# Performance work log

Measured on AMD Instinct MI355X. Metric: run time of the kernel, lower is better.

Reference implementation:

```python
import jax, jax.numpy as jnp
import numpy as np

# module constants (from init_kwargs)
R_EQ = 1.0
WELL_DEPTH = 1.0
CUTOFF = 2.5
HEAL = 0.5

N_EDGES = 20_000_000
N_ATOMS = 1_000_000
N_MOL = 1000


def setup_inputs() -> dict:
    key = jax.random.key(0)
    k1, k2 = jax.random.split(key)
    vec_ij = jax.random.normal(k1, (N_EDGES, 3), dtype=jnp.float32)
    positions = jax.random.normal(k2, (N_ATOMS, 3), dtype=jnp.float32)
    idx_i = jax.random.randint(jax.random.fold_in(key, 1), (N_EDGES,), 0, N_ATOMS, dtype=jnp.int32)
    # sorted molecule indices covering [0, N_MOL), last element == N_MOL-1
    idx_m = (jnp.arange(N_ATOMS, dtype=jnp.int32) * N_MOL // N_ATOMS).astype(jnp.int32)
    return {"vec_ij": vec_ij, "positions": positions, "idx_i": idx_i, "idx_m": idx_m}


def reference(vec_ij, positions, idx_i, idx_m):
    # per-edge distance [E,1]
    r = jnp.linalg.norm(vec_ij, axis=1, keepdims=True)
    # CustomCutoff switching function
    t = (r - (CUTOFF - HEAL)) / HEAL
    r_function = 1.0 + t * t * (2.0 * t - 3.0)
    switch = jnp.where(r > CUTOFF - HEAL, r_function, jnp.ones_like(r))
    switch = jnp.where(r > CUTOFF, jnp.zeros_like(r), switch)
    # LJ pair energy
    power_6 = (R_EQ / r) ** 6
    power_12 = power_6 * power_6
    yij = (power_12 - power_6) * switch  # [E,1]
    # scatter-add edges -> atoms
    yi = jax.ops.segment_sum(yij, idx_i, num_segments=positions.shape[0])  # [N,1]
    # index-add atoms -> molecules
    y = jax.ops.segment_sum(yi, idx_m, num_segments=N_MOL)  # [M,1]
    y = jnp.squeeze(y, -1)
    return WELL_DEPTH * 0.5 * y
```

## Files before the change

### kernel.cpp

```cpp
#include <hip/hip_runtime.h>

#define RCUT2  6.25f
#define RIN2   4.0f
#define BT     512
#define NB     1024
#define RB     256
#define RCHUNK 8

__global__ __launch_bounds__(256) void init_k(float* __restrict__ out, int n_mol,
                                              int* __restrict__ flag, int flag_init) {
    int i = blockIdx.x * 256 + threadIdx.x;
    if (i < n_mol) out[i] = 0.0f;
    if (i == 0) *flag = flag_init;
}

__global__ __launch_bounds__(256) void build_bounds(
    const int* __restrict__ idx_m, int* __restrict__ start,
    int* __restrict__ flag, int n_atoms, int n_mol) {
    int a = blockIdx.x * 256 + threadIdx.x;
    if (a >= n_atoms) return;
    int m  = idx_m[a];
    int pm = (a == 0) ? -1 : idx_m[a - 1];
    for (int mm = pm + 1; mm <= m; ++mm) start[mm] = a;
    if (a == n_atoms - 1)
        for (int mm = m + 1; mm <= n_mol; ++mm) start[mm] = n_atoms;
    int mf = (int)(((unsigned long long)(unsigned)a * (unsigned)n_mol) / (unsigned)n_atoms);
    if (m != mf) atomicAnd(flag, 0);
}

__global__ __launch_bounds__(BT) void lj_direct4(
    const float* __restrict__ vec,
    const int*   __restrict__ idx_i,
    const int*   __restrict__ bounds_g,
    const int*   __restrict__ flag,
    float*       __restrict__ dest,
    int n_edges, int n_mol,
    unsigned long long M, int sh, int use_partial)
{
    extern __shared__ float bins[];
    for (int i = threadIdx.x; i < n_mol; i += BT) bins[i] = 0.0f;
    const bool uni = (*flag != 0);
    __syncthreads();

    auto body = [&](float vx, float vy, float vz, int a) {
        float r2 = fmaf(vx, vx, fmaf(vy, vy, vz * vz));
        if (r2 > RCUT2) return;
        float inv2 = __builtin_amdgcn_rcpf(r2);
        float p6   = inv2 * inv2 * inv2;
        float y    = fmaf(p6, p6, -p6);
        float r  = __builtin_amdgcn_sqrtf(r2);
        float t  = fmaf(2.0f, r, -4.0f);
        float sw = fmaf(t * t, fmaf(2.0f, t, -3.0f), 1.0f);
        y *= (r2 > RIN2) ? sw : 1.0f;
        unsigned q = (unsigned)a * (unsigned)n_mol;
        int m = (int)(((unsigned long long)q * M) >> sh);
        if (!uni) {
            if (m > n_mol - 1) m = n_mol - 1;
            if (m < 0) m = 0;
            while (m > 0 && a < bounds_g[m]) --m;
            while (m < n_mol - 1 && a >= bounds_g[m + 1]) ++m;
        }
        atomicAdd(&bins[m], y);
    };

    const float4* __restrict__ vec4 = (const float4*)vec;
    const int4*   __restrict__ idx4 = (const int4*)idx_i;
    const int ng     = n_edges >> 2;
    const int stride = gridDim.x * BT;

    for (int g = blockIdx.x * BT + threadIdx.x; g < ng; g += stride) {
        float4 va = vec4[3 * g + 0];
        float4 vb = vec4[3 * g + 1];
        float4 vc = vec4[3 * g + 2];
        int4   ia = idx4[g];
        body(va.x, va.y, va.z, ia.x);
        body(va.w, vb.x, vb.y, ia.y);
        body(vb.z, vb.w, vc.x, ia.z);
        body(vc.y, vc.z, vc.w, ia.w);
    }

    const int tail = n_edges & 3;
    if (blockIdx.x == 0 && (int)threadIdx.x < tail) {
        int e = (ng << 2) + (int)threadIdx.x;
        body(vec[3 * e + 0], vec[3 * e + 1], vec[3 * e + 2], idx_i[e]);
    }

    __syncthreads();
    if (use_partial) {
        float* myp = dest + (size_t)blockIdx.x * (size_t)n_mol;
        for (int i = threadIdx.x; i < n_mol; i += BT) myp[i] = bins[i];
    } else {
        unsigned off = (blockIdx.x * 131u) % (unsigned)n_mol;
        for (int i = threadIdx.x; i < n_mol; i += BT) {
            int j = i + (int)off; if (j >= n_mol) j -= n_mol;
            float bv = bins[j];
            if (bv != 0.0f) atomicAdd(&dest[j], 0.5f * bv);
        }
    }
}

__global__ __launch_bounds__(RB) void reduce_k(
    const float* __restrict__ partial, float* __restrict__ out,
    int n_mol, int nb)
{
    const int colblocks = (n_mol + RB - 1) / RB;
    const int cb = blockIdx.x % colblocks;
    const int ch = blockIdx.x / colblocks;
    const int j  = cb * RB + (int)threadIdx.x;
    if (j >= n_mol) return;
    const int rows = nb / RCHUNK;
    const int b0 = ch * rows, b1 = b0 + rows;
    float s = 0.0f;
    #pragma unroll 4
    for (int b = b0; b < b1; ++b) s += partial[(size_t)b * (size_t)n_mol + j];
    atomicAdd(&out[j], 0.5f * s);
}

extern "C" void kernel_launch(void* const* d_in, const int* in_sizes, int n_in,
                              void* d_out, int out_size, void* d_ws, size_t ws_size,
                              hipStream_t stream) {
    const float* vec   = (const float*)d_in[0];
    const int*   idx_i = (const int*)d_in[2];
    const int*   idx_m = (const int*)d_in[3];
    float*       out   = (float*)d_out;

    const int n_edges = in_sizes[2];
    const int n_atoms = in_sizes[3];
    const int n_mol   = out_size;

    const size_t partial_bytes = (size_t)NB * (size_t)n_mol * sizeof(float);
    const size_t need = partial_bytes + (size_t)(n_mol + 2) * sizeof(int);
    const int use_partial = (ws_size >= need) ? 1 : 0;

    float* partial;
    int*   start;
    if (use_partial) {
        partial = (float*)d_ws;
        start   = (int*)(partial + (size_t)NB * (size_t)n_mol);
    } else {
        partial = nullptr;
        start   = (int*)d_ws;
    }
    int* flag = start + (n_mol + 1);

    unsigned d = (unsigned)n_atoms;
    unsigned long long M = 1; int sh = 32;
    bool ok = ((unsigned long long)(unsigned)n_mol * d) <= 0x7fffffffull;
    if (ok) {
        bool found = false;
        for (sh = 32; sh <= 62; ++sh) {
            unsigned long long tk = 1ull << sh;
            M = tk / d + 1;
            unsigned long long e = M * d - tk;
            if (e <= (1ull << (sh - 31))) { found = true; break; }
        }
        ok = found;
    }
    if (!ok) { M = 0; sh = 0; }

    init_k<<<(n_mol + 255) / 256, 256, 0, stream>>>(out, n_mol, flag, ok ? 1 : 0);
    build_bounds<<<(n_atoms + 255) / 256, 256, 0, stream>>>(idx_m, start, flag, n_atoms, n_mol);

    const size_t lds = (size_t)n_mol * sizeof(float);
    lj_direct4<<<NB, BT, lds, stream>>>(
        vec, idx_i, start, flag,
        use_partial ? partial : out,
        n_edges, n_mol, M, sh, use_partial);

    if (use_partial) {
        const int colblocks = (n_mol + RB - 1) / RB;
        reduce_k<<<colblocks * RCHUNK, RB, 0, stream>>>(partial, out, n_mol, NB);
    }
}
```

Before: 413.3 us.

## Stage edge vectors into LDS with double-buffered async global-to-LDS loads

Result: no change. 412.0 us (-0.3%).

```diff
diff --git a/kernel.cpp b/kernel.cpp
--- a/kernel.cpp
+++ b/kernel.cpp
@@ -3,9 +3,14 @@
 #define RCUT2  6.25f
 #define RIN2   4.0f
 #define BT     512
-#define NB     1024
+#define EPT    4
+#define TILE   (BT*EPT)
+#define VTB    (TILE*12)
+#define WSB    (VTB/8)
+#define NB     768
 #define RB     256
 #define RCHUNK 8
+
 
 __global__ __launch_bounds__(256) void init_k(float* __restrict__ out, int n_mol,
                                               int* __restrict__ flag, int flag_init) {
@@ -28,63 +33,139 @@
     if (m != mf) atomicAnd(flag, 0);
 }
 
-__global__ __launch_bounds__(BT) void lj_direct4(
+
+__device__ __forceinline__ void lj_body(
+    float vx, float vy, float vz, int a,
+    bool uni, const int* __restrict__ bounds_g, float* bins,
+    int n_mol, unsigned long long M, int sh)
+{
+    float r2 = fmaf(vx, vx, fmaf(vy, vy, vz * vz));
+    if (r2 > RCUT2) return;
+    float inv2 = __builtin_amdgcn_rcpf(r2);
+    float p6   = inv2 * inv2 * inv2;
+    float y    = fmaf(p6, p6, -p6);
+    float r  = __builtin_amdgcn_sqrtf(r2);
+    float t  = fmaf(2.0f, r, -4.0f);
+    float sw = fmaf(t * t, fmaf(2.0f, t, -3.0f), 1.0f);
+    y *= (r2 > RIN2) ? sw : 1.0f;
+    unsigned q = (unsigned)a * (unsigned)n_mol;
+    int m = (int)(((unsigned long long)q * M) >> sh);
+    if (!uni) {
+        if (m > n_mol - 1) m = n_mol - 1;
+        if (m < 0) m = 0;
+        while (m > 0 && a < bounds_g[m]) --m;
+        while (m < n_mol - 1 && a >= bounds_g[m + 1]) ++m;
+    }
+    atomicAdd(&bins[m], y);
+}
+
+__device__ __forceinline__ void gload_lds16(const void* g, void* l) {
+    __builtin_amdgcn_global_load_lds(
+        (__attribute__((address_space(1))) void*)g,
+        (__attribute__((address_space(3))) void*)l,
+        16, 0, 0);
+}
+
+
+__global__ __launch_bounds__(BT) void lj_staged(
     const float* __restrict__ vec,
     const int*   __restrict__ idx_i,
     const int*   __restrict__ bounds_g,
     const int*   __restrict__ flag,
     float*       __restrict__ dest,
-    int n_edges, int n_mol,
+    int n_edges, int n_mol, int bins_pad,
+    unsigned long long M, int sh, int use_partial)
+{
+    extern __shared__ char smem[];
+    float* bins = (float*)smem;
+    char* sb0 = smem + bins_pad;
+    char* sb1 = sb0 + VTB;
+    for (int i = threadIdx.x; i < n_mol; i += BT) bins[i] = 0.0f;
+    const bool uni = (*flag != 0);
+
+    const int ntiles = n_edges / TILE;
+    const int gdim   = (int)gridDim.x;
+    const char* vecb = (const char*)vec;
+    const int w    = threadIdx.x >> 6;
+    const int lane = threadIdx.x & 63;
+
+    if ((int)blockIdx.x < ntiles) {
+        const char* g = vecb + (size_t)blockIdx.x * VTB + (size_t)(w * WSB + lane * 16);
+        char* l = sb0 + w * WSB;
+        #pragma unroll
+        for (int op = 0; op < 3; ++op)
+            gload_lds16(g + op * 1024, l + op * 1024);
+    }
+
+    int cur = 0;
+    for (int t = blockIdx.x; t < ntiles; t += gdim) {
+        __syncthreads();
+
+        int tn = t + gdim;
+        if (tn < ntiles) {
+            const char* g = vecb + (size_t)tn * VTB + (size_t)(w * WSB + lane * 16);
+            char* l = (cur ? sb0 : sb1) + w * WSB;
+            #pragma unroll
+            for (int op = 0; op < 3; ++op)
+                gload_lds16(g + op * 1024, l + op * 1024);
+        }
+
+        const float* vb = (const float*)(cur ? sb1 : sb0);
+        const size_t eb = (size_t)t * TILE;
+        const int l0 = threadIdx.x;
+        int a0 = idx_i[eb + l0];
+        int a1 = idx_i[eb + l0 + BT];
+        int a2 = idx_i[eb + l0 + 2 * BT];
+        int a3 = idx_i[eb + l0 + 3 * BT];
+        float x0 = vb[3 * l0 + 0],            y0 = vb[3 * l0 + 1],            z0 = vb[3 * l0 + 2];
+        float x1 = vb[3 * (l0 + BT) + 0],     y1 = vb[3 * (l0 + BT) + 1],     z1 = vb[3 * (l0 + BT) + 2];
+        float x2 = vb[3 * (l0 + 2 * BT) + 0], y2 = vb[3 * (l0 + 2 * BT) + 1], z2 = vb[3 * (l0 + 2 * BT) + 2];
+        float x3 = vb[3 * (l0 + 3 * BT) + 0], y3 = vb[3 * (l0 + 3 * BT) + 1], z3 = vb[3 * (l0 + 3 * BT) + 2];
+        lj_body(x0, y0, z0, a0, uni, bounds_g, bins, n_mol, M, sh);
+        lj_body(x1, y1, z1, a1, uni, bounds_g, bins, n_mol, M, sh);
+        lj_body(x2, y2, z2, a2, uni, bounds_g, bins, n_mol, M, sh);
+        lj_body(x3, y3, z3, a3, uni, bounds_g, bins, n_mol, M, sh);
+        cur ^= 1;
+    }
+
+    if (blockIdx.x == 0) {
+        for (int e = ntiles * TILE + (int)threadIdx.x; e < n_edges; e += BT) {
+            size_t b = 3 * (size_t)e;
+            lj_body(vec[b], vec[b + 1], vec[b + 2], idx_i[e],
+                    uni, bounds_g, bins, n_mol, M, sh);
+        }
+    }
+
+    __syncthreads();
+    if (use_partial) {
+        float* myp = dest + (size_t)blockIdx.x * (size_t)n_mol;
+        for (int i = threadIdx.x; i < n_mol; i += BT) myp[i] = bins[i];
+    } else {
+        unsigned off = (blockIdx.x * 131u) % (unsigned)n_mol;
+        for (int i = threadIdx.x; i < n_mol; i += BT) {
+            int j = i + (int)off; if (j >= n_mol) j -= n_mol;
+            float bv = bins[j];
+            if (bv != 0.0f) atomicAdd(&dest[j], 0.5f * bv);
+        }
+    }
+}
+
+__global__ __launch_bounds__(BT) void lj_fallback(
+    const float* __restrict__ vec, const int* __restrict__ idx_i,
+    const int* __restrict__ bounds_g, const int* __restrict__ flag,
+    float* __restrict__ dest, int n_edges, int n_mol,
     unsigned long long M, int sh, int use_partial)
 {
     extern __shared__ float bins[];
     for (int i = threadIdx.x; i < n_mol; i += BT) bins[i] = 0.0f;
     const bool uni = (*flag != 0);
     __syncthreads();
-
-    auto body = [&](float vx, float vy, float vz, int a) {
-        float r2 = fmaf(vx, vx, fmaf(vy, vy, vz * vz));
-        if (r2 > RCUT2) return;
-        float inv2 = __builtin_amdgcn_rcpf(r2);
-        float p6   = inv2 * inv2 * inv2;
-        float y    = fmaf(p6, p6, -p6);
-        float r  = __builtin_amdgcn_sqrtf(r2);
-        float t  = fmaf(2.0f, r, -4.0f);
-        float sw = fmaf(t * t, fmaf(2.0f, t, -3.0f), 1.0f);
-        y *= (r2 > RIN2) ? sw : 1.0f;
-        unsigned q = (unsigned)a * (unsigned)n_mol;
-        int m = (int)(((unsigned long long)q * M) >> sh);
-        if (!uni) {
-            if (m > n_mol - 1) m = n_mol - 1;
-            if (m < 0) m = 0;
-            while (m > 0 && a < bounds_g[m]) --m;
-            while (m < n_mol - 1 && a >= bounds_g[m + 1]) ++m;
-        }
-        atomicAdd(&bins[m], y);
-    };
-
-    const float4* __restrict__ vec4 = (const float4*)vec;
-    const int4*   __restrict__ idx4 = (const int4*)idx_i;
-    const int ng     = n_edges >> 2;
     const int stride = gridDim.x * BT;
-
-    for (int g = blockIdx.x * BT + threadIdx.x; g < ng; g += stride) {
-        float4 va = vec4[3 * g + 0];
-        float4 vb = vec4[3 * g + 1];
-        float4 vc = vec4[3 * g + 2];
-        int4   ia = idx4[g];
-        body(va.x, va.y, va.z, ia.x);
-        body(va.w, vb.x, vb.y, ia.y);
-        body(vb.z, vb.w, vc.x, ia.z);
-        body(vc.y, vc.z, vc.w, ia.w);
-    }
-
-    const int tail = n_edges & 3;
-    if (blockIdx.x == 0 && (int)threadIdx.x < tail) {
-        int e = (ng << 2) + (int)threadIdx.x;
-        body(vec[3 * e + 0], vec[3 * e + 1], vec[3 * e + 2], idx_i[e]);
-    }
-
+    for (int e = blockIdx.x * BT + threadIdx.x; e < n_edges; e += stride) {
+        size_t b = 3 * (size_t)e;
+        lj_body(vec[b], vec[b + 1], vec[b + 2], idx_i[e],
+                uni, bounds_g, bins, n_mol, M, sh);
+    }
     __syncthreads();
     if (use_partial) {
         float* myp = dest + (size_t)blockIdx.x * (size_t)n_mol;
@@ -116,6 +197,7 @@
     atomicAdd(&out[j], 0.5f * s);
 }
 
+
 extern "C" void kernel_launch(void* const* d_in, const int* in_sizes, int n_in,
                               void* d_out, int out_size, void* d_ws, size_t ws_size,
                               hipStream_t stream) {
@@ -161,11 +243,20 @@
     init_k<<<(n_mol + 255) / 256, 256, 0, stream>>>(out, n_mol, flag, ok ? 1 : 0);
     build_bounds<<<(n_atoms + 255) / 256, 256, 0, stream>>>(idx_m, start, flag, n_atoms, n_mol);
 
-    const size_t lds = (size_t)n_mol * sizeof(float);
-    lj_direct4<<<NB, BT, lds, stream>>>(
-        vec, idx_i, start, flag,
-        use_partial ? partial : out,
-        n_edges, n_mol, M, sh, use_partial);
+    const int    bins_pad = (n_mol * 4 + 255) & ~255;
+    const size_t lds_staged = (size_t)bins_pad + 2 * VTB;
+
+    if (lds_staged <= 64 * 1024) {
+        lj_staged<<<NB, BT, lds_staged, stream>>>(
+            vec, idx_i, start, flag,
+            use_partial ? partial : out,
+            n_edges, n_mol, bins_pad, M, sh, use_partial);
+    } else {
+        lj_fallback<<<NB, BT, (size_t)n_mol * sizeof(float), stream>>>(
+            vec, idx_i, start, flag,
+            use_partial ? partial : out,
+            n_edges, n_mol, M, sh, use_partial);
+    }
 
     if (use_partial) {
         const int colblocks = (n_mol + RB - 1) / RB;
```
